# Performance work log

Hardware: AMD Instinct MI355X
Metric: run time of the kernel (lower is better)

## Reference

```python
import jax, jax.numpy as jnp
import numpy as np

TEMPERATURE = 0.07
NEG_INF = -9e15
EPS = 1e-12

def setup_inputs() -> dict:
    key = jax.random.key(0)
    k1, k2 = jax.random.split(key)
    N, D = 8192, 128
    features = jax.random.normal(k1, (N, D), dtype=jnp.float32)
    labels = jax.random.randint(k2, (N,), 0, 16, dtype=jnp.int64)
    return {"features": features, "labels": labels}

def reference(features, labels):
    N = features.shape[0]
    # L2 normalize rows (torch F.normalize: x / max(||x||, eps))
    norm = jnp.linalg.norm(features, axis=1, keepdims=True)
    f = features / jnp.maximum(norm, EPS)
    # [N, N] similarity
    sim = jnp.matmul(f, f.T) / TEMPERATURE
    eye = jnp.eye(N, dtype=bool)
    sim = jnp.where(eye, NEG_INF, sim)
    # positive-pair mask: same label, excluding self
    pos_mask = ((labels[:, None] == labels[None, :]) & ~eye).astype(sim.dtype)
    denom = jnp.exp(sim).sum(axis=1, keepdims=True)  # [N, 1]
    log_prob = sim - jnp.log(denom + EPS)
    loss = -(pos_mask * log_prob).sum(axis=1) / (pos_mask.sum(axis=1) + EPS)
    return loss.mean()
```

## Files before the change

### kernel.cpp

```cpp
#include <hip/hip_runtime.h>
#include <hip/hip_bf16.h>

#define TEMP_INV (1.0f / 0.07f)
#define EPS 1e-12f
#define C_EXP 20.609929155556625f
#define NUM_CLASSES 16
#define CS_BLOCKS 128

#define BM 256
#define BN 128
#define KD 128
#define NCHUNK 8
#define NPART 16

typedef __attribute__((ext_vector_type(4))) float f32x4;
typedef __attribute__((ext_vector_type(8))) short bf16x8;

__device__ __forceinline__ float bf2f(ushort u) {
    unsigned int x = ((unsigned int)u) << 16;
    return __uint_as_float(x);
}

__device__ __forceinline__ const bf16x8* lds_frag(const ushort* base, int r, int slot) {
    int sw = slot ^ (r & 7);
    return reinterpret_cast<const bf16x8*>(
        reinterpret_cast<const char*>(base) + r * 256 + sw * 16);
}

__global__ void normalize_kernel(const float* __restrict__ feat,
                                 ushort* __restrict__ fb,
                                 float* __restrict__ sq,
                                 int N, int D) {
    int wave = (blockIdx.x * blockDim.x + threadIdx.x) >> 6;
    int lane = threadIdx.x & 63;
    if (wave >= N) return;
    const float* row = feat + (size_t)wave * D;
    float s = 0.f;
    for (int k = lane; k < D; k += 64) { float v = row[k]; s += v * v; }
    #pragma unroll
    for (int off = 1; off < 64; off <<= 1) s += __shfl_xor(s, off);
    float scale = 1.0f / fmaxf(sqrtf(s), EPS);
    ushort* orow = fb + (size_t)wave * D;
    float q = 0.f;
    for (int k = lane; k < D; k += 64) {
        __hip_bfloat16 h = __float2bfloat16(row[k] * scale);
        ushort u = *reinterpret_cast<ushort*>(&h);
        orow[k] = u;
        float hv = bf2f(u);
        q += hv * hv;
    }
    #pragma unroll
    for (int off = 1; off < 64; off <<= 1) q += __shfl_xor(q, off);
    if (lane == 0) sq[wave] = q;
}

__global__ __launch_bounds__(256) void classsum_kernel(
    const ushort* __restrict__ fb,
    const int* __restrict__ labels,
    float* __restrict__ g,
    float* __restrict__ cntf,
    int N, int D) {
    __shared__ float lds[2][NUM_CLASSES][128];
    __shared__ float ldc[2][NUM_CLASSES];
    const int d    = threadIdx.x & 127;
    const int half = threadIdx.x >> 7;
    #pragma unroll
    for (int c = 0; c < NUM_CLASSES; c++) lds[half][c][d] = 0.f;
    if (d < NUM_CLASSES) ldc[half][d] = 0.f;
    __syncthreads();

    const int rows_per_block = N / CS_BLOCKS;
    const int half_rows = rows_per_block >> 1;
    const int r0 = blockIdx.x * rows_per_block + half * half_rows;
    for (int r = r0; r < r0 + half_rows; r++) {
        int lab = labels[r];
        lds[half][lab][d] += bf2f(fb[(size_t)r * D + d]);
        if (d == 0) ldc[half][lab] += 1.f;
    }
    __syncthreads();

    for (int c = half; c < NUM_CLASSES; c += 2)
        atomicAdd(&g[c * D + d], lds[0][c][d] + lds[1][c][d]);
    if (threadIdx.x < NUM_CLASSES)
        atomicAdd(&cntf[threadIdx.x], ldc[0][threadIdx.x] + ldc[1][threadIdx.x]);
}

__global__ __launch_bounds__(512, 2) void supcon_denom(
    const ushort* __restrict__ fb,
    float* __restrict__ denom_part,
    int N, int D) {

    __shared__ __align__(16) ushort As[BM * KD];
    __shared__ __align__(16) ushort Bs[2][BN * KD];

    const int tid  = threadIdx.x;
    const int lane = tid & 63;
    const int w    = tid >> 6;
    const int wr   = w >> 1;
    const int wc   = w & 1;
    const int r16  = lane & 15;
    const int g4   = lane >> 4;

    const int rowbase = blockIdx.y * BM;
    const int col0    = blockIdx.x * (BN * NCHUNK);

    {
        const ushort* gA = fb + (size_t)rowbase * KD;
        #pragma unroll
        for (int i = 0; i < 8; i++) {
            int c = i * 512 + tid;
            bf16x8 v = *reinterpret_cast<const bf16x8*>(gA + c * 8);
            int dst = c ^ ((c >> 4) & 7);
            *reinterpret_cast<bf16x8*>(&As[dst * 8]) = v;
        }
        const ushort* gB = fb + (size_t)col0 * KD;
        #pragma unroll
        for (int i = 0; i < 4; i++) {
            int c = i * 512 + tid;
            bf16x8 v = *reinterpret_cast<const bf16x8*>(gB + c * 8);
            int dst = c ^ ((c >> 4) & 7);
            *reinterpret_cast<bf16x8*>(&Bs[0][dst * 8]) = v;
        }
    }
    __syncthreads();

    float pd[4][4];
    #pragma unroll
    for (int m = 0; m < 4; m++)
        #pragma unroll
        for (int i = 0; i < 4; i++) pd[m][i] = 0.f;

    int cur = 0;
    for (int c = 0; c < NCHUNK; c++) {
        bf16x8 pre0, pre1, pre2, pre3;
        if (c + 1 < NCHUNK) {
            const ushort* gB = fb + (size_t)(col0 + (c + 1) * BN) * KD;
            pre0 = *reinterpret_cast<const bf16x8*>(gB + (0 * 512 + tid) * 8);
            pre1 = *reinterpret_cast<const bf16x8*>(gB + (1 * 512 + tid) * 8);
            pre2 = *reinterpret_cast<const bf16x8*>(gB + (2 * 512 + tid) * 8);
            pre3 = *reinterpret_cast<const bf16x8*>(gB + (3 * 512 + tid) * 8);
        }

        f32x4 acc[4][4];
        #pragma unroll
        for (int m = 0; m < 4; m++)
            #pragma unroll
            for (int n = 0; n < 4; n++) acc[m][n] = f32x4{0.f, 0.f, 0.f, 0.f};

        const ushort* bbase = Bs[cur];
        #pragma unroll
        for (int ks = 0; ks < 4; ks++) {
            const int slot = ks * 4 + g4;
            bf16x8 av[4], bv[4];
            #pragma unroll
            for (int m = 0; m < 4; m++)
                av[m] = *lds_frag(As, wr * 64 + m * 16 + r16, slot);
            #pragma unroll
            for (int n = 0; n < 4; n++)
                bv[n] = *lds_frag(bbase, wc * 64 + n * 16 + r16, slot);
            #pragma unroll
            for (int m = 0; m < 4; m++)
                #pragma unroll
                for (int n = 0; n < 4; n++)
                    acc[m][n] = __builtin_amdgcn_mfma_f32_16x16x32_bf16(av[m], bv[n], acc[m][n], 0, 0, 0);
        }

        #pragma unroll
        for (int m = 0; m < 4; m++)
            #pragma unroll
            for (int n = 0; n < 4; n++)
                #pragma unroll
                for (int i = 0; i < 4; i++)
                    pd[m][i] += __builtin_amdgcn_exp2f(acc[m][n][i] * C_EXP);

        if (c + 1 < NCHUNK) {
            ushort* dstb = Bs[cur ^ 1];
            int ch;
            ch = 0 * 512 + tid; *reinterpret_cast<bf16x8*>(&dstb[(ch ^ ((ch >> 4) & 7)) * 8]) = pre0;
            ch = 1 * 512 + tid; *reinterpret_cast<bf16x8*>(&dstb[(ch ^ ((ch >> 4) & 7)) * 8]) = pre1;
            ch = 2 * 512 + tid; *reinterpret_cast<bf16x8*>(&dstb[(ch ^ ((ch >> 4) & 7)) * 8]) = pre2;
            ch = 3 * 512 + tid; *reinterpret_cast<bf16x8*>(&dstb[(ch ^ ((ch >> 4) & 7)) * 8]) = pre3;
        }
        __syncthreads();
        cur ^= 1;
    }

    #pragma unroll
    for (int off = 1; off < 16; off <<= 1)
        #pragma unroll
        for (int m = 0; m < 4; m++)
            #pragma unroll
            for (int i = 0; i < 4; i++)
                pd[m][i] += __shfl_xor(pd[m][i], off);

    if (r16 == 0) {
        const int part = blockIdx.x * 2 + wc;
        #pragma unroll
        for (int m = 0; m < 4; m++)
            #pragma unroll
            for (int i = 0; i < 4; i++) {
                int r = rowbase + wr * 64 + m * 16 + g4 * 4 + i;
                denom_part[(size_t)r * NPART + part] = pd[m][i];
            }
    }
}

__global__ void rowloss_kernel(const ushort* __restrict__ fb,
                               const int* __restrict__ labels,
                               const float* __restrict__ denom_part,
                               const float* __restrict__ sq,
                               const float* __restrict__ g,
                               const float* __restrict__ cntf,
                               float* __restrict__ rowloss,
                               int N, int D) {
    int r    = (blockIdx.x * blockDim.x + threadIdx.x) >> 6;
    int lane = threadIdx.x & 63;
    if (r >= N) return;
    int lab = labels[r];
    const ushort* frow = fb + (size_t)r * D;
    const float*  grow = g + lab * D;
    float p = 0.f;
    for (int k = lane; k < D; k += 64) p += bf2f(frow[k]) * grow[k];
    #pragma unroll
    for (int off = 1; off < 64; off <<= 1) p += __shfl_xor(p, off);

    float dsum = (lane < NPART) ? denom_part[(size_t)r * NPART + lane] : 0.f;
    #pragma unroll
    for (int off = 1; off < NPART; off <<= 1) dsum += __shfl_xor(dsum, off);

    if (lane == 0) {
        float sqr    = sq[r];
        float possum = (p - sqr) * TEMP_INV;
        float cnt    = cntf[lab] - 1.0f;
        float dn     = dsum - __builtin_amdgcn_exp2f(sqr * C_EXP);
        rowloss[r]   = -(possum - cnt * logf(dn + EPS)) / (cnt + EPS);
    }
}

__global__ void reduce_kernel(const float* __restrict__ rowloss,
                              float* __restrict__ out, int N) {
    __shared__ float sdata[16];
    float s = 0.f;
    for (int r = threadIdx.x; r < N; r += blockDim.x) s += rowloss[r];
    #pragma unroll
    for (int off = 1; off < 64; off <<= 1) s += __shfl_xor(s, off);
    int wv = threadIdx.x >> 6;
    if ((threadIdx.x & 63) == 0) sdata[wv] = s;
    __syncthreads();
    if (threadIdx.x == 0) {
        float t = 0.f;
        int nw = (int)(blockDim.x >> 6);
        for (int i = 0; i < nw; i++) t += sdata[i];
        out[0] = t / (float)N;
    }
}

extern "C" void kernel_launch(void* const* d_in, const int* in_sizes, int n_in,
                              void* d_out, int out_size, void* d_ws, size_t ws_size,
                              hipStream_t stream) {
    const float* feat = (const float*)d_in[0];
    const int* labels = (const int*)d_in[1];
    const int N = in_sizes[1];
    const int D = in_sizes[0] / N;

    char* ws = (char*)d_ws;
    ushort* fb = (ushort*)ws;
    size_t off = (size_t)N * D * sizeof(ushort);
    float* g     = (float*)(ws + off);  off += (size_t)NUM_CLASSES * D * sizeof(float);
    float* cntf  = (float*)(ws + off);  off += (size_t)NUM_CLASSES * sizeof(float);
    size_t zbytes = (size_t)(NUM_CLASSES * D + NUM_CLASSES) * sizeof(float);
    float* sq         = (float*)(ws + off); off += (size_t)N * sizeof(float);
    float* rowloss    = (float*)(ws + off); off += (size_t)N * sizeof(float);
    float* denom_part = (float*)(ws + off);

    hipMemsetAsync(g, 0, zbytes, stream);

    normalize_kernel<<<(N + 3) / 4, 256, 0, stream>>>(feat, fb, sq, N, D);
    classsum_kernel<<<CS_BLOCKS, 256, 0, stream>>>(fb, labels, g, cntf, N, D);

    dim3 grid(N / (BN * NCHUNK), N / BM);
    supcon_denom<<<grid, 512, 0, stream>>>(fb, denom_part, N, D);

    rowloss_kernel<<<(N + 3) / 4, 256, 0, stream>>>(fb, labels, denom_part, sq, g, cntf, rowloss, N, D);
    reduce_kernel<<<1, 1024, 0, stream>>>(rowloss, (float*)d_out, N);
}
```

Baseline: 57.54 us.

## Shrink GEMM tiles, replace class-sum atomics with partial reduce, vectorize row kernels

```diff
diff --git a/kernel.cpp b/kernel.cpp
--- a/kernel.cpp
+++ b/kernel.cpp
@@ -7,10 +7,10 @@
 #define NUM_CLASSES 16
 #define CS_BLOCKS 128
 
-#define BM 256
-#define BN 128
+#define BM 128
+#define BN 64
 #define KD 128
-#define NCHUNK 8
+#define NCHUNK 16
 #define NPART 16
 
 typedef __attribute__((ext_vector_type(4))) float f32x4;
@@ -30,36 +30,36 @@
 __global__ void normalize_kernel(const float* __restrict__ feat,
                                  ushort* __restrict__ fb,
                                  float* __restrict__ sq,
-                                 int N, int D) {
-    int wave = (blockIdx.x * blockDim.x + threadIdx.x) >> 6;
+                                 int N) {
+    int r    = (blockIdx.x * blockDim.x + threadIdx.x) >> 6;
     int lane = threadIdx.x & 63;
-    if (wave >= N) return;
-    const float* row = feat + (size_t)wave * D;
-    float s = 0.f;
-    for (int k = lane; k < D; k += 64) { float v = row[k]; s += v * v; }
+    if (r >= N) return;
+    const float2 v = *reinterpret_cast<const float2*>(feat + (size_t)r * KD + lane * 2);
+    float s = v.x * v.x + v.y * v.y;
     #pragma unroll
     for (int off = 1; off < 64; off <<= 1) s += __shfl_xor(s, off);
-    float scale = 1.0f / fmaxf(sqrtf(s), EPS);
-    ushort* orow = fb + (size_t)wave * D;
-    float q = 0.f;
-    for (int k = lane; k < D; k += 64) {
-        __hip_bfloat16 h = __float2bfloat16(row[k] * scale);
-        ushort u = *reinterpret_cast<ushort*>(&h);
-        orow[k] = u;
-        float hv = bf2f(u);
-        q += hv * hv;
-    }
+    const float scale = 1.0f / fmaxf(sqrtf(s), EPS);
+
+    __hip_bfloat16 h0 = __float2bfloat16(v.x * scale);
+    __hip_bfloat16 h1 = __float2bfloat16(v.y * scale);
+    ushort u0 = *reinterpret_cast<ushort*>(&h0);
+    ushort u1 = *reinterpret_cast<ushort*>(&h1);
+    unsigned int pack = (unsigned int)u0 | ((unsigned int)u1 << 16);
+    *reinterpret_cast<unsigned int*>(fb + (size_t)r * KD + lane * 2) = pack;
+
+    float q0 = bf2f(u0), q1 = bf2f(u1);
+    float q = q0 * q0 + q1 * q1;
     #pragma unroll
     for (int off = 1; off < 64; off <<= 1) q += __shfl_xor(q, off);
-    if (lane == 0) sq[wave] = q;
+    if (lane == 0) sq[r] = q;
 }
 
 __global__ __launch_bounds__(256) void classsum_kernel(
     const ushort* __restrict__ fb,
     const int* __restrict__ labels,
-    float* __restrict__ g,
-    float* __restrict__ cntf,
-    int N, int D) {
+    float* __restrict__ g_part,
+    float* __restrict__ cnt_part,
+    int N) {
     __shared__ float lds[2][NUM_CLASSES][128];
     __shared__ float ldc[2][NUM_CLASSES];
     const int d    = threadIdx.x & 127;
@@ -69,26 +69,45 @@
     if (d < NUM_CLASSES) ldc[half][d] = 0.f;
     __syncthreads();
 
-    const int rows_per_block = N / CS_BLOCKS;
-    const int half_rows = rows_per_block >> 1;
-    const int r0 = blockIdx.x * rows_per_block + half * half_rows;
-    for (int r = r0; r < r0 + half_rows; r++) {
+    const int r0 = blockIdx.x * 64 + half * 32;
+    for (int r = r0; r < r0 + 32; r++) {
         int lab = labels[r];
-        lds[half][lab][d] += bf2f(fb[(size_t)r * D + d]);
+        lds[half][lab][d] += bf2f(fb[(size_t)r * KD + d]);
         if (d == 0) ldc[half][lab] += 1.f;
     }
     __syncthreads();
 
     for (int c = half; c < NUM_CLASSES; c += 2)
-        atomicAdd(&g[c * D + d], lds[0][c][d] + lds[1][c][d]);
+        g_part[(size_t)blockIdx.x * 2048 + c * 128 + d] = lds[0][c][d] + lds[1][c][d];
     if (threadIdx.x < NUM_CLASSES)
-        atomicAdd(&cntf[threadIdx.x], ldc[0][threadIdx.x] + ldc[1][threadIdx.x]);
-}
-
-__global__ __launch_bounds__(512, 2) void supcon_denom(
+        cnt_part[blockIdx.x * NUM_CLASSES + threadIdx.x] =
+            ldc[0][threadIdx.x] + ldc[1][threadIdx.x];
+}
+
+__global__ void classreduce_kernel(const float* __restrict__ g_part,
+                                   const float* __restrict__ cnt_part,
+                                   float* __restrict__ g,
+                                   float* __restrict__ cntf) {
+    const int c = blockIdx.x;
+    const int d = threadIdx.x;
+    float acc = 0.f;
+    for (int b = 0; b < CS_BLOCKS; b++)
+        acc += g_part[(size_t)b * 2048 + c * 128 + d];
+    g[c * 128 + d] = acc;
+
+    __shared__ float sc[2];
+    float cv = cnt_part[d * NUM_CLASSES + c];
+    #pragma unroll
+    for (int off = 1; off < 64; off <<= 1) cv += __shfl_xor(cv, off);
+    if ((d & 63) == 0) sc[d >> 6] = cv;
+    __syncthreads();
+    if (d == 0) cntf[c] = sc[0] + sc[1];
+}
+
+__global__ __launch_bounds__(512) void supcon_denom(
     const ushort* __restrict__ fb,
     float* __restrict__ denom_part,
-    int N, int D) {
+    int N) {
 
     __shared__ __align__(16) ushort As[BM * KD];
     __shared__ __align__(16) ushort Bs[2][BN * KD];
@@ -107,7 +126,7 @@
     {
         const ushort* gA = fb + (size_t)rowbase * KD;
         #pragma unroll
-        for (int i = 0; i < 8; i++) {
+        for (int i = 0; i < 4; i++) {
             int c = i * 512 + tid;
             bf16x8 v = *reinterpret_cast<const bf16x8*>(gA + c * 8);
             int dst = c ^ ((c >> 4) & 7);
@@ -115,7 +134,7 @@
         }
         const ushort* gB = fb + (size_t)col0 * KD;
         #pragma unroll
-        for (int i = 0; i < 4; i++) {
+        for (int i = 0; i < 2; i++) {
             int c = i * 512 + tid;
             bf16x8 v = *reinterpret_cast<const bf16x8*>(gB + c * 8);
             int dst = c ^ ((c >> 4) & 7);
@@ -124,51 +143,49 @@
     }
     __syncthreads();
 
-    float pd[4][4];
-    #pragma unroll
-    for (int m = 0; m < 4; m++)
+    float pd[2][4];
+    #pragma unroll
+    for (int m = 0; m < 2; m++)
         #pragma unroll
         for (int i = 0; i < 4; i++) pd[m][i] = 0.f;
 
     int cur = 0;
     for (int c = 0; c < NCHUNK; c++) {
-        bf16x8 pre0, pre1, pre2, pre3;
+        bf16x8 pre0, pre1;
         if (c + 1 < NCHUNK) {
             const ushort* gB = fb + (size_t)(col0 + (c + 1) * BN) * KD;
             pre0 = *reinterpret_cast<const bf16x8*>(gB + (0 * 512 + tid) * 8);
             pre1 = *reinterpret_cast<const bf16x8*>(gB + (1 * 512 + tid) * 8);
-            pre2 = *reinterpret_cast<const bf16x8*>(gB + (2 * 512 + tid) * 8);
-            pre3 = *reinterpret_cast<const bf16x8*>(gB + (3 * 512 + tid) * 8);
-        }
-
-        f32x4 acc[4][4];
-        #pragma unroll
-        for (int m = 0; m < 4; m++)
-            #pragma unroll
-            for (int n = 0; n < 4; n++) acc[m][n] = f32x4{0.f, 0.f, 0.f, 0.f};
+        }
+
+        f32x4 acc[2][2];
+        #pragma unroll
+        for (int m = 0; m < 2; m++)
+            #pragma unroll
+            for (int n = 0; n < 2; n++) acc[m][n] = f32x4{0.f, 0.f, 0.f, 0.f};
 
         const ushort* bbase = Bs[cur];
         #pragma unroll
         for (int ks = 0; ks < 4; ks++) {
             const int slot = ks * 4 + g4;
-            bf16x8 av[4], bv[4];
-            #pragma unroll
-            for (int m = 0; m < 4; m++)
-                av[m] = *lds_frag(As, wr * 64 + m * 16 + r16, slot);
-            #pragma unroll
-            for (int n = 0; n < 4; n++)
-                bv[n] = *lds_frag(bbase, wc * 64 + n * 16 + r16, slot);
-            #pragma unroll
-            for (int m = 0; m < 4; m++)
+            bf16x8 av[2], bv[2];
+            #pragma unroll
+            for (int m = 0; m < 2; m++)
+                av[m] = *lds_frag(As, wr * 32 + m * 16 + r16, slot);
+            #pragma unroll
+            for (int n = 0; n < 2; n++)
+                bv[n] = *lds_frag(bbase, wc * 32 + n * 16 + r16, slot);
+            #pragma unroll
+            for (int m = 0; m < 2; m++)
                 #pragma unroll
-                for (int n = 0; n < 4; n++)
+                for (int n = 0; n < 2; n++)
                     acc[m][n] = __builtin_amdgcn_mfma_f32_16x16x32_bf16(av[m], bv[n], acc[m][n], 0, 0, 0);
         }
 
         #pragma unroll
-        for (int m = 0; m < 4; m++)
-            #pragma unroll
-            for (int n = 0; n < 4; n++)
+        for (int m = 0; m < 2; m++)
+            #pragma unroll
+            for (int n = 0; n < 2; n++)
                 #pragma unroll
                 for (int i = 0; i < 4; i++)
                     pd[m][i] += __builtin_amdgcn_exp2f(acc[m][n][i] * C_EXP);
@@ -178,8 +195,6 @@
             int ch;
             ch = 0 * 512 + tid; *reinterpret_cast<bf16x8*>(&dstb[(ch ^ ((ch >> 4) & 7)) * 8]) = pre0;
             ch = 1 * 512 + tid; *reinterpret_cast<bf16x8*>(&dstb[(ch ^ ((ch >> 4) & 7)) * 8]) = pre1;
-            ch = 2 * 512 + tid; *reinterpret_cast<bf16x8*>(&dstb[(ch ^ ((ch >> 4) & 7)) * 8]) = pre2;
-            ch = 3 * 512 + tid; *reinterpret_cast<bf16x8*>(&dstb[(ch ^ ((ch >> 4) & 7)) * 8]) = pre3;
         }
         __syncthreads();
         cur ^= 1;
@@ -188,7 +203,7 @@
     #pragma unroll
     for (int off = 1; off < 16; off <<= 1)
         #pragma unroll
-        for (int m = 0; m < 4; m++)
+        for (int m = 0; m < 2; m++)
             #pragma unroll
             for (int i = 0; i < 4; i++)
                 pd[m][i] += __shfl_xor(pd[m][i], off);
@@ -196,10 +211,10 @@
     if (r16 == 0) {
         const int part = blockIdx.x * 2 + wc;
         #pragma unroll
-        for (int m = 0; m < 4; m++)
+        for (int m = 0; m < 2; m++)
             #pragma unroll
             for (int i = 0; i < 4; i++) {
-                int r = rowbase + wr * 64 + m * 16 + g4 * 4 + i;
+                int r = rowbase + wr * 32 + m * 16 + g4 * 4 + i;
                 denom_part[(size_t)r * NPART + part] = pd[m][i];
             }
     }
@@ -212,15 +227,16 @@
                                const float* __restrict__ g,
                                const float* __restrict__ cntf,
                                float* __restrict__ rowloss,
-                               int N, int D) {
+                               int N) {
     int r    = (blockIdx.x * blockDim.x + threadIdx.x) >> 6;
     int lane = threadIdx.x & 63;
     if (r >= N) return;
     int lab = labels[r];
-    const ushort* frow = fb + (size_t)r * D;
-    const float*  grow = g + lab * D;
-    float p = 0.f;
-    for (int k = lane; k < D; k += 64) p += bf2f(frow[k]) * grow[k];
+    unsigned int pk = *reinterpret_cast<const unsigned int*>(fb + (size_t)r * KD + lane * 2);
+    float f0 = bf2f((ushort)(pk & 0xffff));
+    float f1 = bf2f((ushort)(pk >> 16));
+    const float2 gv = *reinterpret_cast<const float2*>(g + lab * 128 + lane * 2);
+    float p = f0 * gv.x + f1 * gv.y;
     #pragma unroll
     for (int off = 1; off < 64; off <<= 1) p += __shfl_xor(p, off);
 
@@ -261,26 +277,25 @@
     const float* feat = (const float*)d_in[0];
     const int* labels = (const int*)d_in[1];
     const int N = in_sizes[1];
-    const int D = in_sizes[0] / N;
 
     char* ws = (char*)d_ws;
-    ushort* fb = (ushort*)ws;
-    size_t off = (size_t)N * D * sizeof(ushort);
-    float* g     = (float*)(ws + off);  off += (size_t)NUM_CLASSES * D * sizeof(float);
-    float* cntf  = (float*)(ws + off);  off += (size_t)NUM_CLASSES * sizeof(float);
-    size_t zbytes = (size_t)(NUM_CLASSES * D + NUM_CLASSES) * sizeof(float);
-    float* sq         = (float*)(ws + off); off += (size_t)N * sizeof(float);
-    float* rowloss    = (float*)(ws + off); off += (size_t)N * sizeof(float);
-    float* denom_part = (float*)(ws + off);
-
-    hipMemsetAsync(g, 0, zbytes, stream);
-
-    normalize_kernel<<<(N + 3) / 4, 256, 0, stream>>>(feat, fb, sq, N, D);
-    classsum_kernel<<<CS_BLOCKS, 256, 0, stream>>>(fb, labels, g, cntf, N, D);
+    size_t off = 0;
+    ushort* fb        = (ushort*)(ws + off); off += (size_t)N * KD * sizeof(ushort);
+    float* sq         = (float*)(ws + off);  off += (size_t)N * sizeof(float);
+    float* g_part     = (float*)(ws + off);  off += (size_t)CS_BLOCKS * NUM_CLASSES * KD * sizeof(float);
+    float* cnt_part   = (float*)(ws + off);  off += (size_t)CS_BLOCKS * NUM_CLASSES * sizeof(float);
+    float* g          = (float*)(ws + off);  off += (size_t)NUM_CLASSES * KD * sizeof(float);
+    float* cntf       = (float*)(ws + off);  off += (size_t)NUM_CLASSES * sizeof(float);
+    float* denom_part = (float*)(ws + off);  off += (size_t)N * NPART * sizeof(float);
+    float* rowloss    = (float*)(ws + off);
+
+    normalize_kernel<<<(N + 3) / 4, 256, 0, stream>>>(feat, fb, sq, N);
+    classsum_kernel<<<CS_BLOCKS, 256, 0, stream>>>(fb, labels, g_part, cnt_part, N);
+    classreduce_kernel<<<NUM_CLASSES, 128, 0, stream>>>(g_part, cnt_part, g, cntf);
 
     dim3 grid(N / (BN * NCHUNK), N / BM);
-    supcon_denom<<<grid, 512, 0, stream>>>(fb, denom_part, N, D);
-
-    rowloss_kernel<<<(N + 3) / 4, 256, 0, stream>>>(fb, labels, denom_part, sq, g, cntf, rowloss, N, D);
+    supcon_denom<<<grid, 512, 0, stream>>>(fb, denom_part, N);
+
+    rowloss_kernel<<<(N + 3) / 4, 256, 0, stream>>>(fb, labels, denom_part, sq, g, cntf, rowloss, N);
     reduce_kernel<<<1, 1024, 0, stream>>>(rowloss, (float*)d_out, N);
 }
```

After: 62.61 us. +8.8%, slower.
